# Kernel tuning notes

Hardware: AMD Instinct MI355X
Metric: run time of the kernel (lower is better)

## Reference

```python
import jax, jax.numpy as jnp
import numpy as np

S, B, E, H, AW = 4096, 2, 768, 12, 512  # seq, batch, embed, heads, attention_window


def _longformer_local_attn(query, Wq, bq, Wk, bk, Wv, bv):
    # query: [S, B, E] (seq-first, as in the torch module); returns [S, B, E]
    S_, B_, E_ = query.shape
    H_ = H
    D = E_ // H_
    W = AW // 2  # one-sided window (HF Longformer uses window//2 each side)
    x = query.transpose(1, 0, 2)  # [B, S, E]

    q = (x @ Wq + bq).reshape(B_, S_, H_, D) * (1.0 / jnp.sqrt(jnp.asarray(D, x.dtype)))
    k = (x @ Wk + bk).reshape(B_, S_, H_, D)
    v = (x @ Wv + bv).reshape(B_, S_, H_, D)

    nc = S_ // W  # number of query chunks of size W
    # pad keys/values by W on each side so every chunk sees a 3W key window
    kp = jnp.pad(k, ((0, 0), (W, W), (0, 0), (0, 0)))
    vp = jnp.pad(v, ((0, 0), (W, W), (0, 0), (0, 0)))
    # padded-coordinate indices of the 3W key window for each chunk: [nc, 3W]
    idx = jnp.arange(nc)[:, None] * W + jnp.arange(3 * W)[None, :]
    kc = kp[:, idx]  # [B, nc, 3W, H, D]
    vc = vp[:, idx]  # [B, nc, 3W, H, D]
    qc = q.reshape(B_, nc, W, H_, D)

    # banded scores: [B, H, nc, W, 3W]
    scores = jnp.einsum('bcqhd,bckhd->bhcqk', qc, kc)

    # mask: within-band (|rel| <= W) and inside the real sequence
    rel = (jnp.arange(3 * W) - W)[None, :] - jnp.arange(W)[:, None]  # [W, 3W]
    band = jnp.abs(rel) <= W
    abs_k = idx - W  # absolute key index, [nc, 3W]
    in_seq = (abs_k >= 0) & (abs_k < S_)
    mask = band[None, :, :] & in_seq[:, None, :]  # [nc, W, 3W]

    scores = jnp.where(mask[None, None], scores, -jnp.inf)
    attn = jax.nn.softmax(scores, axis=-1)
    out = jnp.einsum('bhcqk,bckhd->bcqhd', attn, vc).reshape(B_, S_, E_)
    return out.transpose(1, 0, 2)  # back to [S, B, E]


def setup_inputs() -> dict:
    key = jax.random.key(0)
    ks = jax.random.split(key, 4)
    scale = 0.02
    return {
        'query': jax.random.normal(ks[0], (S, B, E), jnp.float32),
        'Wq': jax.random.normal(ks[1], (E, E), jnp.float32) * scale,
        'bq': jnp.zeros((E,), jnp.float32),
        'Wk': jax.random.normal(ks[2], (E, E), jnp.float32) * scale,
        'bk': jnp.zeros((E,), jnp.float32),
        'Wv': jax.random.normal(ks[3], (E, E), jnp.float32) * scale,
        'bv': jnp.zeros((E,), jnp.float32),
    }


def reference(query, Wq, bq, Wk, bk, Wv, bv):
    # dropout is identity in eval mode; no global tokens (global mask defaults to zeros)
    return _longformer_local_attn(query, Wq, bq, Wk, bk, Wv, bv)
```

## Files before the change

kernel.cpp:

```cpp
#include <hip/hip_runtime.h>

#define S_ 4096
#define B_ 2
#define E_ 768
#define H_ 12
#define D_ 64

typedef __attribute__((ext_vector_type(8))) short short8;
typedef __attribute__((ext_vector_type(4))) float f32x4;
typedef unsigned short u16;
typedef unsigned int u32;

__device__ __forceinline__ u16 f2bf(float f) {
  union { float f; u32 u; } v; v.f = f;
  u32 r = v.u + 0x7FFFu + ((v.u >> 16) & 1u);
  return (u16)(r >> 16);
}

__device__ __forceinline__ void gl_lds16(const void* g, void* l) {
  __builtin_amdgcn_global_load_lds((const __attribute__((address_space(1))) u32*)g,
                                   (__attribute__((address_space(3))) u32*)l, 16, 0, 0);
}

__global__ __launch_bounds__(192) void k_convert_x(const float* __restrict__ q,
                                                   u16* __restrict__ x) {
  int m = blockIdx.x;
  int e = threadIdx.x * 4;
  int b = m >> 12, s = m & 4095;
  const float4 v = *(const float4*)&q[((s << 1) + b) * 768 + e];
  ushort4 o;
  o.x = f2bf(v.x); o.y = f2bf(v.y); o.z = f2bf(v.z); o.w = f2bf(v.w);
  *(ushort4*)&x[m * 768 + e] = o;
}

__global__ __launch_bounds__(256) void k_transpose_w(const float* __restrict__ w0,
                                                     const float* __restrict__ w1,
                                                     const float* __restrict__ w2,
                                                     u16* __restrict__ wt) {
  __shared__ float tile[32][33];
  const float* w = blockIdx.z == 0 ? w0 : (blockIdx.z == 1 ? w1 : w2);
  int k0 = blockIdx.x * 32, n0 = blockIdx.y * 32;
  int tx = threadIdx.x & 31, ty = threadIdx.x >> 5;
#pragma unroll
  for (int i = 0; i < 4; i++)
    tile[ty + i * 8][tx] = w[(k0 + ty + i * 8) * 768 + n0 + tx];
  __syncthreads();
  u16* o = wt + blockIdx.z * 768 * 768;
#pragma unroll
  for (int i = 0; i < 4; i++)
    o[(n0 + ty + i * 8) * 768 + k0 + tx] = f2bf(tile[tx][ty + i * 8]);
}

__global__ __launch_bounds__(256) void k_gemm_qkv(
    const u16* __restrict__ x, const u16* __restrict__ wt,
    const float* __restrict__ bq, const float* __restrict__ bk,
    const float* __restrict__ bv,
    u16* __restrict__ qb, u16* __restrict__ kb, u16* __restrict__ vt) {
  __shared__ __align__(16) u16 smem[18432];
  const int tid = threadIdx.x;
  const int lane = tid & 63, wave = tid >> 6;
  const int bid = blockIdx.x;
  const int xcd = bid & 7, idx = bid >> 3;
  const int m_l = idx / 18, rem = idx % 18;
  const int n_i = rem / 3, z = rem % 3;
  const int m0 = (xcd * 8 + m_l) * 128, n0 = n_i * 128;
  const u16* wz = wt + z * 768 * 768;
  const int wr = wave >> 1, wc = wave & 1;
  const int l15 = lane & 15, lg = lane >> 4;

  f32x4 acc[4][4] = {};

  auto stage = [&](int buf, int kt) {
#pragma unroll
    for (int c = 0; c < 2; c++) {
      int ci = c * 256 + tid;
      int row = ci >> 2, cp = ci & 3;
      gl_lds16(&x[(size_t)(m0 + row) * 768 + kt + cp * 8],
               &smem[buf * 4096 + (c * 256 + wave * 64) * 8]);
      gl_lds16(&wz[(size_t)(n0 + row) * 768 + kt + cp * 8],
               &smem[8192 + buf * 4096 + (c * 256 + wave * 64) * 8]);
    }
  };

  stage(0, 0);
  __syncthreads();
  for (int t = 0; t < 24; t++) {
    const int buf = t & 1;
    if (t < 23) stage(buf ^ 1, (t + 1) * 32);
    short8 a[4], b[4];
#pragma unroll
    for (int mf = 0; mf < 4; mf++)
      a[mf] = *(const short8*)&smem[buf * 4096 + (wr * 64 + mf * 16 + l15) * 32 + lg * 8];
#pragma unroll
    for (int nf = 0; nf < 4; nf++)
      b[nf] = *(const short8*)&smem[8192 + buf * 4096 + (wc * 64 + nf * 16 + l15) * 32 + lg * 8];
#pragma unroll
    for (int mf = 0; mf < 4; mf++)
#pragma unroll
      for (int nf = 0; nf < 4; nf++)
        acc[mf][nf] = __builtin_amdgcn_mfma_f32_16x16x32_bf16(a[mf], b[nf], acc[mf][nf], 0, 0, 0);
    __syncthreads();
  }

  u16* ep = &smem[wave * 4608];
  const float* bias_p = (z == 0) ? bq : (z == 1 ? bk : bv);
  const int r8 = lane >> 3, cn = lane & 7;
  if (z < 2) {
    const float sc = (z == 0) ? 0.125f : 1.0f;
#pragma unroll
    for (int nf = 0; nf < 4; nf++) {
      int n = n0 + wc * 64 + nf * 16 + l15;
      float bias = bias_p[n];
#pragma unroll
      for (int mf = 0; mf < 4; mf++)
#pragma unroll
        for (int r = 0; r < 4; r++)
          ep[(mf * 16 + lg * 4 + r) * 72 + nf * 16 + l15] =
              f2bf((acc[mf][nf][r] + bias) * sc);
    }
    __syncthreads();
    u16* t = (z == 0) ? qb : kb;
#pragma unroll
    for (int i = 0; i < 8; i++) {
      int rl = i * 8 + r8;
      short8 v = *(const short8*)&ep[rl * 72 + cn * 8];
      *(short8*)&t[(size_t)(m0 + wr * 64 + rl) * 768 + n0 + wc * 64 + cn * 8] = v;
    }
  } else {
#pragma unroll
    for (int nf = 0; nf < 4; nf++) {
      int n = n0 + wc * 64 + nf * 16 + l15;
      float bias = bias_p[n];
#pragma unroll
      for (int mf = 0; mf < 4; mf++) {
        ushort4 pk;
        pk.x = f2bf(acc[mf][nf][0] + bias);
        pk.y = f2bf(acc[mf][nf][1] + bias);
        pk.z = f2bf(acc[mf][nf][2] + bias);
        pk.w = f2bf(acc[mf][nf][3] + bias);
        *(ushort4*)&ep[(nf * 16 + l15) * 72 + mf * 16 + lg * 4] = pk;
      }
    }
    __syncthreads();
    const int bb = m0 >> 12, srow = m0 & 4095;
#pragma unroll
    for (int i = 0; i < 8; i++) {
      int nl = i * 8 + r8;
      int n = n0 + wc * 64 + nl;
      int h = n >> 6, d = n & 63;
      short8 v = *(const short8*)&ep[nl * 72 + cn * 8];
      *(short8*)&vt[(((size_t)(bb * 12 + h) * 64 + d) << 12) + srow + wr * 64 + cn * 8] = v;
    }
  }
}

__global__ __launch_bounds__(256) void k_attn(const u16* __restrict__ qb,
                                              const u16* __restrict__ kb,
                                              const u16* __restrict__ vt,
                                              float* __restrict__ out) {
  __shared__ __align__(16) u16 Ks[2][64 * 64];
  __shared__ __align__(16) u16 Vs[2][64 * 64];
  __shared__ __align__(16) u16 pl[4][32 * 72];
  const int tid = threadIdx.x;
  const int lane = tid & 63, wave = tid >> 6;
  const int l15 = lane & 15, lg = lane >> 4;

  const int bid = blockIdx.x;
  const int xcd = bid & 7, i = bid >> 3;
  const int pair = xcd * 3 + (i >> 5);
  const int chunk = i & 31;
  const int b = pair / 12, h = pair % 12;
  const int s0 = chunk * 128;
  const int q0 = s0 + wave * 32;

  short8 qf[2][2];
#pragma unroll
  for (int mf = 0; mf < 2; mf++)
#pragma unroll
    for (int ks = 0; ks < 2; ks++)
      qf[mf][ks] = *(const short8*)&qb[(size_t)((b << 12) + q0 + mf * 16 + l15) * 768 +
                                       h * 64 + ks * 32 + lg * 8];

  f32x4 o[2][4] = {};
  float lsum[2][4] = {};

  int t0 = s0 - 256; if (t0 < 0) t0 = 0;
  int t1 = s0 + 320; if (t1 > 4032) t1 = 4032;

  auto stage = [&](int buf, int kb0) {
#pragma unroll
    for (int c = 0; c < 2; c++) {
      int ci = c * 256 + tid;
      int row = ci >> 3, cc = ci & 7;
      int sc = cc ^ (row & 7);
      gl_lds16(&kb[(size_t)((b << 12) + kb0 + row) * 768 + h * 64 + sc * 8],
               &Ks[buf][(c * 256 + wave * 64) * 8]);
      gl_lds16(&vt[((size_t)((b * 12 + h) * 64 + row) << 12) + kb0 + sc * 8],
               &Vs[buf][(c * 256 + wave * 64) * 8]);
    }
  };

  stage(0, t0);
  int buf = 0;
  for (int kb0 = t0; kb0 <= t1; kb0 += 64) {
    if (kb0 + 64 <= t1) stage(buf ^ 1, kb0 + 64);
    __syncthreads();
    const bool act = (kb0 + 63 >= q0 - 256) && (kb0 <= q0 + 31 + 256);
    if (act) {
      f32x4 sf[2][4] = {};
#pragma unroll
      for (int ks = 0; ks < 2; ks++) {
        short8 bkf[4];
#pragma unroll
        for (int nf = 0; nf < 4; nf++) {
          int row = nf * 16 + l15;
          bkf[nf] = *(const short8*)&Ks[buf][row * 64 + (((ks * 4 + lg) ^ (row & 7)) * 8)];
        }
#pragma unroll
        for (int mf = 0; mf < 2; mf++)
#pragma unroll
          for (int nf = 0; nf < 4; nf++)
            sf[mf][nf] = __builtin_amdgcn_mfma_f32_16x16x32_bf16(qf[mf][ks], bkf[nf], sf[mf][nf], 0, 0, 0);
      }
      if (kb0 < q0 - 192 || kb0 > q0 + 192) {
#pragma unroll
        for (int mf = 0; mf < 2; mf++)
#pragma unroll
          for (int nf = 0; nf < 4; nf++) {
            int kj = kb0 + nf * 16 + l15;
#pragma unroll
            for (int r = 0; r < 4; r++) {
              int qi = q0 + mf * 16 + lg * 4 + r;
              if ((unsigned)(kj - qi + 256) > 512u) sf[mf][nf][r] = -3e38f;
            }
          }
      }
      u16* plw = pl[wave];
#pragma unroll
      for (int mf = 0; mf < 2; mf++)
#pragma unroll
        for (int nf = 0; nf < 4; nf++)
#pragma unroll
          for (int r = 0; r < 4; r++) {
            float p = __expf(sf[mf][nf][r]);
            lsum[mf][r] += p;
            plw[(mf * 16 + lg * 4 + r) * 72 + nf * 16 + l15] = f2bf(p);
          }
      short8 pa[2][2];
#pragma unroll
      for (int mf = 0; mf < 2; mf++)
#pragma unroll
        for (int ks = 0; ks < 2; ks++)
          pa[mf][ks] = *(const short8*)&plw[(mf * 16 + l15) * 72 + ks * 32 + lg * 8];
#pragma unroll
      for (int ks = 0; ks < 2; ks++) {
        short8 bvf[4];
#pragma unroll
        for (int df = 0; df < 4; df++) {
          int row = df * 16 + l15;
          bvf[df] = *(const short8*)&Vs[buf][row * 64 + (((ks * 4 + lg) ^ (row & 7)) * 8)];
        }
#pragma unroll
        for (int mf = 0; mf < 2; mf++)
#pragma unroll
          for (int df = 0; df < 4; df++)
            o[mf][df] = __builtin_amdgcn_mfma_f32_16x16x32_bf16(pa[mf][ks], bvf[df], o[mf][df], 0, 0, 0);
      }
    }
    __syncthreads();
    buf ^= 1;
  }

#pragma unroll
  for (int mf = 0; mf < 2; mf++)
#pragma unroll
    for (int r = 0; r < 4; r++) {
      float l = lsum[mf][r];
      l += __shfl_xor(l, 1); l += __shfl_xor(l, 2);
      l += __shfl_xor(l, 4); l += __shfl_xor(l, 8);
      lsum[mf][r] = l;
    }

#pragma unroll
  for (int mf = 0; mf < 2; mf++)
#pragma unroll
    for (int df = 0; df < 4; df++)
#pragma unroll
      for (int r = 0; r < 4; r++) {
        int s = q0 + mf * 16 + lg * 4 + r;
        out[(size_t)(s * 2 + b) * 768 + h * 64 + df * 16 + l15] =
            o[mf][df][r] / lsum[mf][r];
      }
}

extern "C" void kernel_launch(void* const* d_in, const int* in_sizes, int n_in,
                              void* d_out, int out_size, void* d_ws, size_t ws_size,
                              hipStream_t stream) {
  const float* query = (const float*)d_in[0];
  const float* Wq = (const float*)d_in[1];
  const float* bq = (const float*)d_in[2];
  const float* Wk = (const float*)d_in[3];
  const float* bk = (const float*)d_in[4];
  const float* Wv = (const float*)d_in[5];
  const float* bv = (const float*)d_in[6];
  float* out = (float*)d_out;

  char* ws = (char*)d_ws;
  size_t off = 0;
  auto alloc = [&](size_t bytes) {
    void* p = ws + off;
    off = (off + bytes + 255) & ~(size_t)255;
    return p;
  };
  u16* x  = (u16*)alloc((size_t)8192 * 768 * 2);
  u16* wt = (u16*)alloc((size_t)3 * 768 * 768 * 2);
  u16* qb = (u16*)alloc((size_t)8192 * 768 * 2);
  u16* kb = (u16*)alloc((size_t)8192 * 768 * 2);
  u16* vt = (u16*)alloc((size_t)8192 * 768 * 2);

  hipLaunchKernelGGL(k_convert_x, dim3(8192), dim3(192), 0, stream, query, x);
  hipLaunchKernelGGL(k_transpose_w, dim3(24, 24, 3), dim3(256), 0, stream, Wq, Wk, Wv, wt);
  hipLaunchKernelGGL(k_gemm_qkv, dim3(1152), dim3(256), 0, stream,
                     x, wt, bq, bk, bv, qb, kb, vt);
  hipLaunchKernelGGL(k_attn, dim3(768), dim3(256), 0, stream, qb, kb, vt, out);
}
```

Baseline: 173.0 us.

## Enlarge QKV GEMM tile to 256x128 with XOR-swizzled LDS layout

```diff
diff --git a/kernel.cpp b/kernel.cpp
--- a/kernel.cpp
+++ b/kernel.cpp
@@ -51,51 +51,62 @@
     o[(n0 + ty + i * 8) * 768 + k0 + tx] = f2bf(tile[tx][ty + i * 8]);
 }
 
-__global__ __launch_bounds__(256) void k_gemm_qkv(
+__global__ __launch_bounds__(256, 2) void k_gemm_qkv(
     const u16* __restrict__ x, const u16* __restrict__ wt,
     const float* __restrict__ bq, const float* __restrict__ bk,
     const float* __restrict__ bv,
     u16* __restrict__ qb, u16* __restrict__ kb, u16* __restrict__ vt) {
-  __shared__ __align__(16) u16 smem[18432];
+  __shared__ __align__(16) u16 smem[24576];
   const int tid = threadIdx.x;
   const int lane = tid & 63, wave = tid >> 6;
+  const int wm = wave >> 1, wn = wave & 1;
+  const int l15 = lane & 15, lg = lane >> 4;
+
   const int bid = blockIdx.x;
   const int xcd = bid & 7, idx = bid >> 3;
-  const int m_l = idx / 18, rem = idx % 18;
-  const int n_i = rem / 3, z = rem % 3;
-  const int m0 = (xcd * 8 + m_l) * 128, n0 = n_i * 128;
-  const u16* wz = wt + z * 768 * 768;
-  const int wr = wave >> 1, wc = wave & 1;
-  const int l15 = lane & 15, lg = lane >> 4;
-
-  f32x4 acc[4][4] = {};
+  const int m0 = (xcd * 4 + idx / 18) * 256;
+  const int n0g = (idx % 18) * 128;
+  const int z = n0g / 768, j0 = n0g % 768;
+  const u16* wz = wt + (size_t)z * 768 * 768;
+
+  f32x4 acc[8][4] = {};
 
   auto stage = [&](int buf, int kt) {
+#pragma unroll
+    for (int c = 0; c < 4; c++) {
+      int ci = c * 256 + tid;
+      int row = ci >> 2, cp = ci & 3;
+      int sc = cp ^ ((row >> 1) & 3);
+      gl_lds16(&x[(size_t)(m0 + row) * 768 + kt + sc * 8],
+               &smem[buf * 12288 + (c * 256 + wave * 64) * 8]);
+    }
 #pragma unroll
     for (int c = 0; c < 2; c++) {
       int ci = c * 256 + tid;
       int row = ci >> 2, cp = ci & 3;
-      gl_lds16(&x[(size_t)(m0 + row) * 768 + kt + cp * 8],
-               &smem[buf * 4096 + (c * 256 + wave * 64) * 8]);
-      gl_lds16(&wz[(size_t)(n0 + row) * 768 + kt + cp * 8],
-               &smem[8192 + buf * 4096 + (c * 256 + wave * 64) * 8]);
+      int sc = cp ^ ((row >> 1) & 3);
+      gl_lds16(&wz[(size_t)(j0 + row) * 768 + kt + sc * 8],
+               &smem[buf * 12288 + 8192 + (c * 256 + wave * 64) * 8]);
     }
   };
 
   stage(0, 0);
   __syncthreads();
+  const int kc = lg ^ ((l15 >> 1) & 3);
   for (int t = 0; t < 24; t++) {
     const int buf = t & 1;
     if (t < 23) stage(buf ^ 1, (t + 1) * 32);
-    short8 a[4], b[4];
-#pragma unroll
-    for (int mf = 0; mf < 4; mf++)
-      a[mf] = *(const short8*)&smem[buf * 4096 + (wr * 64 + mf * 16 + l15) * 32 + lg * 8];
+    short8 a[8], b[4];
+#pragma unroll
+    for (int mf = 0; mf < 8; mf++)
+      a[mf] = *(const short8*)&smem[buf * 12288 +
+                                    (wm * 128 + mf * 16 + l15) * 32 + kc * 8];
 #pragma unroll
     for (int nf = 0; nf < 4; nf++)
-      b[nf] = *(const short8*)&smem[8192 + buf * 4096 + (wc * 64 + nf * 16 + l15) * 32 + lg * 8];
-#pragma unroll
-    for (int mf = 0; mf < 4; mf++)
+      b[nf] = *(const short8*)&smem[buf * 12288 + 8192 +
+                                    (wn * 64 + nf * 16 + l15) * 32 + kc * 8];
+#pragma unroll
+    for (int mf = 0; mf < 8; mf++)
 #pragma unroll
       for (int nf = 0; nf < 4; nf++)
         acc[mf][nf] = __builtin_amdgcn_mfma_f32_16x16x32_bf16(a[mf], b[nf], acc[mf][nf], 0, 0, 0);
@@ -104,52 +115,63 @@
 
   u16* ep = &smem[wave * 4608];
   const float* bias_p = (z == 0) ? bq : (z == 1 ? bk : bv);
+  const float sc_ = (z == 0) ? 0.125f : 1.0f;
   const int r8 = lane >> 3, cn = lane & 7;
   if (z < 2) {
-    const float sc = (z == 0) ? 0.125f : 1.0f;
-#pragma unroll
-    for (int nf = 0; nf < 4; nf++) {
-      int n = n0 + wc * 64 + nf * 16 + l15;
-      float bias = bias_p[n];
-#pragma unroll
-      for (int mf = 0; mf < 4; mf++)
-#pragma unroll
-        for (int r = 0; r < 4; r++)
-          ep[(mf * 16 + lg * 4 + r) * 72 + nf * 16 + l15] =
-              f2bf((acc[mf][nf][r] + bias) * sc);
-    }
-    __syncthreads();
     u16* t = (z == 0) ? qb : kb;
 #pragma unroll
-    for (int i = 0; i < 8; i++) {
-      int rl = i * 8 + r8;
-      short8 v = *(const short8*)&ep[rl * 72 + cn * 8];
-      *(short8*)&t[(size_t)(m0 + wr * 64 + rl) * 768 + n0 + wc * 64 + cn * 8] = v;
+    for (int hh = 0; hh < 2; hh++) {
+      __syncthreads();
+#pragma unroll
+      for (int mfl = 0; mfl < 4; mfl++) {
+        int mf = hh * 4 + mfl;
+#pragma unroll
+        for (int nf = 0; nf < 4; nf++) {
+          float bias = bias_p[j0 + wn * 64 + nf * 16 + l15];
+#pragma unroll
+          for (int r = 0; r < 4; r++)
+            ep[(mfl * 16 + lg * 4 + r) * 72 + nf * 16 + l15] =
+                f2bf((acc[mf][nf][r] + bias) * sc_);
+        }
+      }
+      __syncthreads();
+#pragma unroll
+      for (int i = 0; i < 8; i++) {
+        int rl = i * 8 + r8;
+        short8 v = *(const short8*)&ep[rl * 72 + cn * 8];
+        *(short8*)&t[(size_t)(m0 + wm * 128 + hh * 64 + rl) * 768 +
+                     j0 + wn * 64 + cn * 8] = v;
+      }
     }
   } else {
-#pragma unroll
-    for (int nf = 0; nf < 4; nf++) {
-      int n = n0 + wc * 64 + nf * 16 + l15;
-      float bias = bias_p[n];
-#pragma unroll
-      for (int mf = 0; mf < 4; mf++) {
-        ushort4 pk;
-        pk.x = f2bf(acc[mf][nf][0] + bias);
-        pk.y = f2bf(acc[mf][nf][1] + bias);
-        pk.z = f2bf(acc[mf][nf][2] + bias);
-        pk.w = f2bf(acc[mf][nf][3] + bias);
-        *(ushort4*)&ep[(nf * 16 + l15) * 72 + mf * 16 + lg * 4] = pk;
-      }
-    }
-    __syncthreads();
     const int bb = m0 >> 12, srow = m0 & 4095;
 #pragma unroll
-    for (int i = 0; i < 8; i++) {
-      int nl = i * 8 + r8;
-      int n = n0 + wc * 64 + nl;
-      int h = n >> 6, d = n & 63;
-      short8 v = *(const short8*)&ep[nl * 72 + cn * 8];
-      *(short8*)&vt[(((size_t)(bb * 12 + h) * 64 + d) << 12) + srow + wr * 64 + cn * 8] = v;
+    for (int hh = 0; hh < 2; hh++) {
+      __syncthreads();
+#pragma unroll
+      for (int nf = 0; nf < 4; nf++) {
+        float bias = bias_p[j0 + wn * 64 + nf * 16 + l15];
+#pragma unroll
+        for (int mfl = 0; mfl < 4; mfl++) {
+          int mf = hh * 4 + mfl;
+          ushort4 pk;
+          pk.x = f2bf(acc[mf][nf][0] + bias);
+          pk.y = f2bf(acc[mf][nf][1] + bias);
+          pk.z = f2bf(acc[mf][nf][2] + bias);
+          pk.w = f2bf(acc[mf][nf][3] + bias);
+          *(ushort4*)&ep[(nf * 16 + l15) * 72 + mfl * 16 + lg * 4] = pk;
+        }
+      }
+      __syncthreads();
+#pragma unroll
+      for (int i = 0; i < 8; i++) {
+        int nl = i * 8 + r8;
+        int n = j0 + wn * 64 + nl;
+        int h = n >> 6, d = n & 63;
+        short8 v = *(const short8*)&ep[nl * 72 + cn * 8];
+        *(short8*)&vt[(((size_t)(bb * 12 + h) * 64 + d) << 12) +
+                      srow + wm * 128 + hh * 64 + cn * 8] = v;
+      }
     }
   }
 }
@@ -320,7 +342,7 @@
 
   hipLaunchKernelGGL(k_convert_x, dim3(8192), dim3(192), 0, stream, query, x);
   hipLaunchKernelGGL(k_transpose_w, dim3(24, 24, 3), dim3(256), 0, stream, Wq, Wk, Wv, wt);
-  hipLaunchKernelGGL(k_gemm_qkv, dim3(1152), dim3(256), 0, stream,
+  hipLaunchKernelGGL(k_gemm_qkv, dim3(576), dim3(256), 0, stream,
                      x, wt, bq, bk, bv, qb, kb, vt);
   hipLaunchKernelGGL(k_attn, dim3(768), dim3(256), 0, stream, qb, kb, vt, out);
 }
```

Result: no change. 170.1 us (-1.7%).
